# Optimization experiments

Hardware: AMD Instinct MI355X
Metric: run time of the kernel (lower is better)

## Reference

```python
import jax, jax.numpy as jnp
import numpy as np

N = 4096      # num nodes
E = 131072    # num edges
D = 128       # embed dim (in=out)
HID = 16      # kan hidden dim
G, K = 4, 3   # KAN grid_size / spline_order (GCN + FFN kans)
GA, KA = 2, 1 # attention KANLinear grid_size / spline_order
H, HD = 8, 16 # heads, head_dim

def make_grid(in_f, g, k):
    h = 2.0 / g
    pts = (np.arange(-k, g + k + 1) * h - 1.0).astype(np.float32)  # [g+2k+1]
    return jnp.asarray(np.tile(pts[None, :], (in_f, 1)))            # [in_f, g+2k+1]

GRID_D = make_grid(D, G, K)
GRID_H = make_grid(HID, G, K)
GRID_A = make_grid(D, GA, KA)

def b_splines(x, grid, k):
    # x: [n, in] -> B-spline bases [n, in, g+k] via Cox-de-Boor recursion
    x = x[:, :, None]
    g = grid[None]
    bases = ((x >= g[..., :-1]) & (x < g[..., 1:])).astype(x.dtype)
    for j in range(1, k + 1):
        bases = ((x - g[..., :-(j + 1)]) / (g[..., j:-1] - g[..., :-(j + 1)]) * bases[..., :-1]
                 + (g[..., j + 1:] - x) / (g[..., j + 1:] - g[..., 1:-j]) * bases[..., 1:])
    return bases

def kan_lin(x, bw, sw, grid, k, use_silu):
    base = jax.nn.silu(x) if use_silu else x
    return base @ bw.T + jnp.einsum('nig,oig->no', b_splines(x, grid, k), sw)

def ekan2(x, bw1, sw1, bw2, sw2):
    # eKAN with layers_hidden=[D, HID, D], SiLU base activation
    h = kan_lin(x, bw1, sw1, GRID_D, K, True)
    return kan_lin(h, bw2, sw2, GRID_H, K, True)

def layer_norm(h, s, b):
    m = jnp.mean(h, axis=-1, keepdims=True)
    v = jnp.var(h, axis=-1, keepdims=True)
    return (h - m) * jax.lax.rsqrt(v + 1e-5) * s + b

def setup_inputs() -> dict:
    key = jax.random.key(0)
    ks = jax.random.split(key, 20)
    r = lambda i, shape: jax.random.normal(ks[i], shape, jnp.float32) * 0.1
    return dict(
        x=jax.random.normal(ks[0], (N, D), jnp.float32),
        edge_index=jax.random.randint(ks[1], (2, E), 0, N),
        gcn_bw1=r(2, (HID, D)), gcn_sw1=r(3, (HID, D, G + K)),
        gcn_bw2=r(4, (D, HID)), gcn_sw2=r(5, (D, HID, G + K)),
        q_bw=r(6, (D, D)), q_sw=r(7, (D, D, GA + KA)),
        k_bw=r(8, (D, D)), k_sw=r(9, (D, D, GA + KA)),
        v_bw=r(10, (D, D)), v_sw=r(11, (D, D, GA + KA)),
        ffn_bw1=r(12, (HID, D)), ffn_sw1=r(13, (HID, D, G + K)),
        ffn_bw2=r(14, (D, HID)), ffn_sw2=r(15, (D, HID, G + K)),
        ln1_s=jnp.ones(D), ln1_b=jnp.zeros(D),
        ln2_s=jnp.ones(D), ln2_b=jnp.zeros(D),
        ln3_s=jnp.ones(D), ln3_b=jnp.zeros(D),
    )

def reference(x, edge_index, gcn_bw1, gcn_sw1, gcn_bw2, gcn_sw2,
              q_bw, q_sw, k_bw, k_sw, v_bw, v_sw,
              ffn_bw1, ffn_sw1, ffn_bw2, ffn_sw2,
              ln1_s, ln1_b, ln2_s, ln2_b, ln3_s, ln3_b):
    n = x.shape[0]
    # ---- local GCN-KAN branch: KAN(A_hat x) ----
    loops = jnp.arange(n)
    row = jnp.concatenate([edge_index[0], loops])  # sources (+ self-loops)
    col = jnp.concatenate([edge_index[1], loops])  # targets
    w = jnp.ones(row.shape[0], x.dtype)
    deg = jax.ops.segment_sum(w, row, num_segments=n)
    dis = jnp.where(deg > 0, deg ** -0.5, 0.0)
    norm = dis[row] * w * dis[col]
    agg = jax.ops.segment_sum(norm[:, None] * x[row], col, num_segments=n)  # [n, D]
    h_local = ekan2(agg, gcn_bw1, gcn_sw1, gcn_bw2, gcn_sw2)
    h_local = layer_norm(x + h_local, ln1_s, ln1_b)
    # ---- global KAN multi-head attention branch ----
    Q = kan_lin(x, q_bw, q_sw, GRID_A, KA, False).reshape(n, H, HD)
    Kv = kan_lin(x, k_bw, k_sw, GRID_A, KA, False).reshape(n, H, HD)
    V = kan_lin(x, v_bw, v_sw, GRID_A, KA, False).reshape(n, H, HD)
    scores = jnp.einsum('nhd,mhd->hnm', Q, Kv) / np.sqrt(HD)  # [H, n, n]
    attn = jax.nn.softmax(scores, axis=-1)
    h_attn = jnp.einsum('hnm,mhd->nhd', attn, V).reshape(n, D)
    h_attn = layer_norm(x + h_attn, ln2_s, ln2_b)
    # ---- combine + KAN feed-forward ----
    h = h_local + h_attn
    out = layer_norm(h + ekan2(h, ffn_bw1, ffn_sw1, ffn_bw2, ffn_sw2), ln3_s, ln3_b)
    return out
```

## Files before the change

### kernel.cpp

```cpp
#include <hip/hip_runtime.h>

typedef unsigned short u16;
typedef unsigned int u32;

#define D_ 128
#define HID_ 16
#define NH_ 8
#define HD_ 16
#define PSTRIDE 17

#define WE_W1G 0
#define WE_W2G 16384
#define WE_W1F 32768
#define WE_W2F 49152
#define WE_TOTAL 65536

#define KROW 24
#define VROW 136
#define PROW 40
#define HROW 136
#define AROW 1032
#define HVROW 132

#define QSCALE 0.3606737602222409f

typedef __attribute__((ext_vector_type(8))) short bfrag;
typedef __attribute__((ext_vector_type(4))) float ffrag;

#if defined(__has_builtin)
#if __has_builtin(__builtin_amdgcn_exp2f)
#define EXP2F(x) __builtin_amdgcn_exp2f(x)
#endif
#endif
#ifndef EXP2F
#define EXP2F(x) exp2f(x)
#endif


__device__ __forceinline__ float bf2f(u16 u) {
    union { u32 i; float f; } v; v.i = ((u32)u) << 16; return v.f;
}
__device__ __forceinline__ u16 f2bf(float f) {
    u32 x = __float_as_uint(f);
    u32 r = (x + 0x7fffu + ((x >> 16) & 1u)) >> 16;
    return (u16)r;
}
__device__ __forceinline__ float rdf(const void* p, int i, bool bf) {
    return bf ? bf2f(((const u16*)p)[i]) : ((const float*)p)[i];
}

__device__ __forceinline__ u32 probe_stat(const u16* p) {
    for (int i = 0; i < 128; i++) {
        u16 u = p[i];
        int e = (u >> 7) & 0xFF;
        int m = u & 0x7F;
        bool zero = (e == 0) && (m == 0);
        bool sane = zero || (e >= 97 && e <= 147);
        if (!sane) return 0u;
    }
    return 1u;
}

__global__ __launch_bounds__(256) void k_detect(const void* x,
                         const void* gbw1, const void* gsw1, const void* gbw2, const void* gsw2,
                         const void* qbw, const void* qsw, const void* kbw, const void* ksw,
                         const void* vbw, const void* vsw,
                         const void* fbw1, const void* fsw1, const void* fbw2, const void* fsw2,
                         const void* l1s, const void* l1b, const void* l2s, const void* l2b,
                         const void* l3s, const void* l3b,
                         u32* flags, int* __restrict__ cnt3, int N) {
    int t = threadIdx.x;
    const void* ptrs[21] = {x, gbw1, gsw1, gbw2, gsw2, qbw, qsw, kbw, ksw, vbw, vsw,
                            fbw1, fsw1, fbw2, fsw2, l1s, l1b, l2s, l2b, l3s, l3b};
    if (t < 21) {
        u32 f = 0;
        if (t == 15 || t == 17 || t == 19) {
            f = (((const u32*)ptrs[t])[0] != 0x3F800000u) ? 1u : 0u;
        } else if (t == 16 || t == 18 || t == 20) {
            f = 0;
        } else {
            f = probe_stat((const u16*)ptrs[t]);
        }
        flags[t] = f;
    }
    __syncthreads();
    if (t == 16 || t == 18 || t == 20) flags[t] = flags[t - 1];
    int tot = 3 * N;
    for (int i = t; i < tot; i += 256) cnt3[i] = 0;
}

__device__ __forceinline__ float cub_seg(float s) {
    if (s < 0.0f || s >= 4.0f) return 0.0f;
    if (s < 1.0f) return s * s * s * (1.0f / 6.0f);
    if (s < 2.0f) { float r = s - 1.0f; return (1.0f + 3.0f * r + 3.0f * r * r - 3.0f * r * r * r) * (1.0f / 6.0f); }
    if (s < 3.0f) { float r = s - 2.0f; return (4.0f - 6.0f * r * r + 3.0f * r * r * r) * (1.0f / 6.0f); }
    float q = 4.0f - s; return q * q * q * (1.0f / 6.0f);
}
__device__ __forceinline__ float lin_seg(float s) {
    if (s < 0.0f || s >= 2.0f) return 0.0f;
    return (s < 1.0f) ? s : (2.0f - s);
}

__device__ __forceinline__ uint4 feat8(float a) {
    float si = a / (1.0f + __expf(-a));
    float u = (a + 2.5f) * 2.0f;
    float b0 = cub_seg(u), b1 = cub_seg(u - 1.0f), b2 = cub_seg(u - 2.0f), b3 = cub_seg(u - 3.0f);
    float b4 = cub_seg(u - 4.0f), b5 = cub_seg(u - 5.0f), b6 = cub_seg(u - 6.0f);
    uint4 r;
    r.x = (u32)f2bf(si) | ((u32)f2bf(b0) << 16);
    r.y = (u32)f2bf(b1) | ((u32)f2bf(b2) << 16);
    r.z = (u32)f2bf(b3) | ((u32)f2bf(b4) << 16);
    r.w = (u32)f2bf(b5) | ((u32)f2bf(b6) << 16);
    return r;
}

__global__ __launch_bounds__(256) void k_setup(const void* __restrict__ x,
        const void* l1s, const void* l1b, const void* l2s,
        const void* l2b, const void* l3s, const void* l3b,
        const void* gbw1, const void* gsw1, const void* gbw2, const void* gsw2,
        const void* fbw1, const void* fsw1, const void* fbw2, const void* fsw2,
        const void* qbw, const void* qsw, const void* kbw, const void* ksw,
        const void* vbw, const void* vsw,
        const int* __restrict__ ei,
        const u32* __restrict__ flags,
        float* __restrict__ xin, float* __restrict__ lnp,
        u16* __restrict__ F,
        u16* __restrict__ Web, u16* __restrict__ Wb,
        int* __restrict__ cnt, int* __restrict__ degi,
        int N, int E) {
    int b = blockIdx.x;
    int convB = ((N * D_ + 768) + 255) >> 8;
    if (b < convB) {
        int i = b * 256 + threadIdx.x;
        if (i < N * D_) {
            float xv = rdf(x, i, flags[0] != 0);
            xin[i] = xv;
            float u = xv + 2.0f;
            u32 lo = (u32)f2bf(xv) | ((u32)f2bf(lin_seg(u)) << 16);
            u32 hi = (u32)f2bf(lin_seg(u - 1.0f)) | ((u32)f2bf(lin_seg(u - 2.0f)) << 16);
            ((uint2*)F)[i] = make_uint2(lo, hi);
        } else if (i < N * D_ + 768) {
            int j = i - N * D_;
            int sel = j >> 7, k = j & 127;
            const void* p = sel == 0 ? l1s : sel == 1 ? l1b : sel == 2 ? l2s
                         : sel == 3 ? l2b : sel == 4 ? l3s : l3b;
            lnp[j] = rdf(p, k, flags[15 + sel] != 0);
        }
    } else if (b < convB + 224) {
        int t = (b - convB) * 256 + threadIdx.x;
        if (t < 8192) {
            int seg = t >> 11, i = t & 2047;
            const void* bw = seg == 0 ? gbw1 : seg == 1 ? gbw2 : seg == 2 ? fbw1 : fbw2;
            const void* sw = seg == 0 ? gsw1 : seg == 1 ? gsw2 : seg == 2 ? fsw1 : fsw2;
            int fb = seg == 0 ? 1 : seg == 1 ? 3 : seg == 2 ? 11 : 13;
            bool bwbf = flags[fb] != 0, swbf = flags[fb + 1] != 0;
            u16* dst = Web + (size_t)seg * 16384 + (size_t)i * 8;
            dst[0] = f2bf(rdf(bw, i, bwbf));
#pragma unroll
            for (int g = 0; g < 7; g++) dst[1 + g] = f2bf(rdf(sw, i * 7 + g, swbf));
        } else if (t < 8192 + 49152) {
            int uu = t - 8192;
            int seg = uu >> 14, i = uu & 16383;
            const void* bw = seg == 0 ? qbw : seg == 1 ? kbw : vbw;
            const void* sw = seg == 0 ? qsw : seg == 1 ? ksw : vsw;
            int fb = 5 + seg * 2;
            bool bwbf = flags[fb] != 0, swbf = flags[fb + 1] != 0;
            float sc = (seg == 0) ? QSCALE : 1.0f;
            u16* dst = Wb + (size_t)seg * 65536 + (size_t)i * 4;
            dst[0] = f2bf(rdf(bw, i, bwbf) * sc);
#pragma unroll
            for (int g = 0; g < 3; g++) dst[1 + g] = f2bf(rdf(sw, i * 3 + g, swbf) * sc);
        }
    } else {
        int e = (b - convB - 224) * 256 + threadIdx.x;
        if (e < E) {
            atomicAdd(&degi[ei[e]], 1);
            atomicAdd(&cnt[ei[E + e]], 1);
        }
    }
}

__global__ __launch_bounds__(1024) void k_scan(const int* __restrict__ cnt,
                                               const int* __restrict__ degi,
                                               int* __restrict__ rowptr,
                                               float* __restrict__ dis, int N) {
    __shared__ int ws[16];
    int t = threadIdx.x;
    int base = t * 4;
    int a[4];
#pragma unroll
    for (int k = 0; k < 4; k++) a[k] = (base + k < N) ? cnt[base + k] : 0;
    int loc = a[0] + a[1] + a[2] + a[3];
    int pre = loc;
#pragma unroll
    for (int off = 1; off < 64; off <<= 1) {
        int v = __shfl_up(pre, off, 64);
        if ((t & 63) >= off) pre += v;
    }
    if ((t & 63) == 63) ws[t >> 6] = pre;
    __syncthreads();
    if (t < 64) {
        int v = (t < 16) ? ws[t] : 0;
#pragma unroll
        for (int off = 1; off < 16; off <<= 1) {
            int u = __shfl_up(v, off, 64);
            if (t >= off) v += u;
        }
        if (t < 16) ws[t] = v;
    }
    __syncthreads();
    int ex = pre - loc + ((t >= 64) ? ws[(t >> 6) - 1] : 0);
    int run = ex;
#pragma unroll
    for (int k = 0; k < 4; k++) {
        if (base + k < N) rowptr[base + k] = run;
        run += a[k];
    }
    if (t == 1023) rowptr[N] = ws[15];
#pragma unroll
    for (int k = 0; k < 4; k++)
        if (base + k < N) dis[base + k] = rsqrtf((float)degi[base + k] + 1.0f);
}

__global__ void k_fill(const int* __restrict__ ei, const int* __restrict__ rowptr,
                       int* __restrict__ fill, int* __restrict__ elist, int E) {
    int e = blockIdx.x * 256 + threadIdx.x;
    if (e < E) {
        int r = ei[e], c = ei[E + e];
        int pos = rowptr[c] + atomicAdd(&fill[c], 1);
        elist[pos] = r;
    }
}

__global__ __launch_bounds__(128) void k_gcn(const int* __restrict__ rowptr,
        const int* __restrict__ elist, const float* __restrict__ dis,
        const float* __restrict__ xin, u16* __restrict__ Afeat) {
    int c = blockIdx.x, t = threadIdx.x;
    __shared__ int ids[128];
    __shared__ float wsh[128];
    int beg = rowptr[c], end = rowptr[c + 1];
    float a0 = 0.0f, a1 = 0.0f, a2 = 0.0f, a3 = 0.0f;
    for (int j0 = beg; j0 < end; j0 += 128) {
        int cc = min(128, end - j0);
        __syncthreads();
        if (t < cc) {
            int rr = elist[j0 + t];
            ids[t] = rr;
            wsh[t] = dis[rr];
        }
        __syncthreads();
        int j = 0;
        for (; j + 4 <= cc; j += 4) {
            a0 += wsh[j]     * xin[(size_t)ids[j]     * D_ + t];
            a1 += wsh[j + 1] * xin[(size_t)ids[j + 1] * D_ + t];
            a2 += wsh[j + 2] * xin[(size_t)ids[j + 2] * D_ + t];
            a3 += wsh[j + 3] * xin[(size_t)ids[j + 3] * D_ + t];
        }
        for (; j < cc; j++) a0 += wsh[j] * xin[(size_t)ids[j] * D_ + t];
    }
    float dc = dis[c];
    float a = dc * (((a0 + a1) + (a2 + a3)) + dc * xin[(size_t)c * D_ + t]);
    ((uint4*)Afeat)[(size_t)c * D_ + t] = feat8(a);
}

#define EKAN_G1(APTR, ASTR, W1B) \
    if (ww == 0) { \
        const u16* ar = (APTR) + (size_t)l15 * (ASTR) + quad * 8; \
        const u16* br = (W1B) + (size_t)l15 * 1024 + quad * 8; \
        ffrag c0 = {0,0,0,0}, c1 = {0,0,0,0}, c2 = {0,0,0,0}, c3 = {0,0,0,0}; \
        for (int ks = 0; ks < 256; ks += 32) { \
            c0 = __builtin_amdgcn_mfma_f32_16x16x32_bf16(*(const bfrag*)(ar + ks),       *(const bfrag*)(br + ks),       c0, 0, 0, 0); \
            c1 = __builtin_amdgcn_mfma_f32_16x16x32_bf16(*(const bfrag*)(ar + 256 + ks), *(const bfrag*)(br + 256 + ks), c1, 0, 0, 0); \
            c2 = __builtin_amdgcn_mfma_f32_16x16x32_bf16(*(const bfrag*)(ar + 512 + ks), *(const bfrag*)(br + 512 + ks), c2, 0, 0, 0); \
            c3 = __builtin_amdgcn_mfma_f32_16x16x32_bf16(*(const bfrag*)(ar + 768 + ks), *(const bfrag*)(br + 768 + ks), c3, 0, 0, 0); \
        } \
        float e0 = (c0.x + c1.x) + (c2.x + c3.x); \
        float e1 = (c0.y + c1.y) + (c2.y + c3.y); \
        float e2 = (c0.z + c1.z) + (c2.z + c3.z); \
        float e3 = (c0.w + c1.w) + (c2.w + c3.w); \
        { uint4 fv = feat8(e0); *(uint4*)(&hfL[(quad * 4 + 0) * HROW + l15 * 8]) = fv; } \
        { uint4 fv = feat8(e1); *(uint4*)(&hfL[(quad * 4 + 1) * HROW + l15 * 8]) = fv; } \
        { uint4 fv = feat8(e2); *(uint4*)(&hfL[(quad * 4 + 2) * HROW + l15 * 8]) = fv; } \
        { uint4 fv = feat8(e3); *(uint4*)(&hfL[(quad * 4 + 3) * HROW + l15 * 8]) = fv; } \
    }

#define EK_TGET(RR, COMP, V0, V1, RES0EXPR, RES1EXPR) { \
    int row = quad * 4 + RR; \
    float r0 = (RES0EXPR); \
    float r1 = (RES1EXPR); \
    V0 = a0.COMP + r0; V1 = a1.COMP + r1; \
    float s1 = V0 + V1, s2 = V0 * V0 + V1 * V1; \
    s1 += __shfl_xor(s1, 1, 64); s2 += __shfl_xor(s2, 1, 64); \
    s1 += __shfl_xor(s1, 2, 64); s2 += __shfl_xor(s2, 2, 64); \
    s1 += __shfl_xor(s1, 4, 64); s2 += __shfl_xor(s2, 4, 64); \
    s1 += __shfl_xor(s1, 8, 64); s2 += __shfl_xor(s2, 8, 64); \
    if (l15 == 0) { redS[ww * 16 + row] = s1; redS[64 + ww * 16 + row] = s2; } }

#define EK_TOUT(RR, V0, V1, OUTP, BFO) { \
    int row = quad * 4 + RR; \
    float s1 = (redS[row] + redS[16 + row]) + (redS[32 + row] + redS[48 + row]); \
    float s2 = (redS[64 + row] + redS[80 + row]) + (redS[96 + row] + redS[112 + row]); \
    float mean = s1 * 0.0078125f; \
    float var = s2 * 0.0078125f - mean * mean; \
    float rs = rsqrtf(var + 1e-5f); \
    float y0 = (V0 - mean) * rs * ls0 + lb0; \
    float y1 = (V1 - mean) * rs * ls1 + lb1; \
    int node = node0 + row; \
    if (BFO) { \
        u16* ob = (u16*)(OUTP) + (size_t)node * 128; \
        ob[c0i] = f2bf(y0); ob[c1i] = f2bf(y1); \
    } else { \
        float* ob = (float*)(OUTP) + (size_t)node * 128; \
        ob[c0i] = y0; ob[c1i] = y1; \
    } }

#define EKAN_G2LN(W2B, LNS, LNB, RES0EXPR, RES1EXPR, OUTP, BFO) { \
    const u16* b0 = (W2B) + (size_t)l15 * 128 + quad * 8 + (size_t)(2 * ww) * 2048; \
    ffrag a0 = {0,0,0,0}, a1 = {0,0,0,0}; \
    for (int ks = 0; ks < 128; ks += 32) { \
        bfrag af = *(const bfrag*)(&hfL[l15 * HROW + quad * 8 + ks]); \
        a0 = __builtin_amdgcn_mfma_f32_16x16x32_bf16(af, *(const bfrag*)(b0 + ks),        a0, 0, 0, 0); \
        a1 = __builtin_amdgcn_mfma_f32_16x16x32_bf16(af, *(const bfrag*)(b0 + 2048 + ks), a1, 0, 0, 0); \
    } \
    int c0i = 32 * ww + l15, c1i = c0i + 16; \
    float ls0 = (LNS)[c0i], lb0 = (LNB)[c0i]; \
    float ls1 = (LNS)[c1i], lb1 = (LNB)[c1i]; \
    float v0r0, v0r1, v0r2, v0r3, v1r0, v1r1, v1r2, v1r3; \
    EK_TGET(0, x, v0r0, v1r0, RES0EXPR, RES1EXPR) \
    EK_TGET(1, y, v0r1, v1r1, RES0EXPR, RES1EXPR) \
    EK_TGET(2, z, v0r2, v1r2, RES0EXPR, RES1EXPR) \
    EK_TGET(3, w, v0r3, v1r3, RES0EXPR, RES1EXPR) \
    __syncthreads(); \
    EK_TOUT(0, v0r0, v1r0, OUTP, BFO) \
    EK_TOUT(1, v0r1, v1r1, OUTP, BFO) \
    EK_TOUT(2, v0r2, v1r2, OUTP, BFO) \
    EK_TOUT(3, v0r3, v1r3, OUTP, BFO) }

__global__ __launch_bounds__(256) void k_ekan4(const u16* __restrict__ A,
        const u16* __restrict__ W1b, const u16* __restrict__ W2b,
        const float* __restrict__ resid,
        const float* __restrict__ lns, const float* __restrict__ lnb,
        float* __restrict__ outp, int N) {
    __shared__ u16 hfL[16 * HROW];
    __shared__ float redS[128];
    int mt = blockIdx.x, t = threadIdx.x;
    int ww = t >> 6, lane = t & 63, quad = lane >> 4, l15 = lane & 15;
    int node0 = mt * 16;
    const u16* Ab = A + (size_t)node0 * 1024;
    EKAN_G1(Ab, 1024, W1b)
    __syncthreads();
    EKAN_G2LN(W2b, lns, lnb,
              resid[(size_t)(node0 + row) * 128 + c0i],
              resid[(size_t)(node0 + row) * 128 + c1i],
              outp, false)
    (void)lane;
}

#define QKV_STORE(ACC, TL) { \
    int col = cg * 48 + (TL) * 16 + l15; \
    int mat = col >> 7, idx = col & 127; \
    u16* dstb = (mat == 0) ? Qb : (mat == 1) ? Kb : Vb; \
    size_t base = (size_t)(idx >> 4) * N * HD_ + (size_t)(idx & 15); \
    dstb[base + (size_t)(rowb + 0) * HD_] = f2bf(ACC.x); \
    dstb[base + (size_t)(rowb + 1) * HD_] = f2bf(ACC.y); \
    dstb[base + (size_t)(rowb + 2) * HD_] = f2bf(ACC.z); \
    dstb[base + (size_t)(rowb + 3) * HD_] = f2bf(ACC.w); \
}

__global__ __launch_bounds__(64) void k_qkv5(const u16* __restrict__ F,
        const u16* __restrict__ Wb,
        u16* __restrict__ Qb, u16* __restrict__ Kb, u16* __restrict__ Vb, int N) {
    int mt = blockIdx.x, cg = blockIdx.y;
    int lane = threadIdx.x, quad = lane >> 4, l15 = lane & 15;
    const u16* arow = F + (size_t)(mt * 16 + l15) * 512 + quad * 8;
    const u16* b0r = Wb + (size_t)(cg * 48 + l15) * 512 + quad * 8;
    const u16* b1r = b0r + 16 * 512;
    const u16* b2r = b0r + 32 * 512;
    ffrag a0 = {0, 0, 0, 0}, a1 = {0, 0, 0, 0}, a2 = {0, 0, 0, 0};
#pragma unroll
    for (int ks = 0; ks < 512; ks += 32) {
        bfrag af = *(const bfrag*)(arow + ks);
        bfrag bf0 = *(const bfrag*)(b0r + ks);
        bfrag bf1 = *(const bfrag*)(b1r + ks);
        bfrag bf2 = *(const bfrag*)(b2r + ks);
        a0 = __builtin_amdgcn_mfma_f32_16x16x32_bf16(af, bf0, a0, 0, 0, 0);
        a1 = __builtin_amdgcn_mfma_f32_16x16x32_bf16(af, bf1, a1, 0, 0, 0);
        a2 = __builtin_amdgcn_mfma_f32_16x16x32_bf16(af, bf2, a2, 0, 0, 0);
    }
    int rowb = mt * 16 + quad * 4;
    QKV_STORE(a0, 0)
    QKV_STORE(a1, 1)
    QKV_STORE(a2, 2)
}

#define ATTN_SCORE(QF, LACC, PBT) { \
    ffrag zz = {0.0f, 0.0f, 0.0f, 0.0f}; \
    ffrag s0 = __builtin_amdgcn_mfma_f32_16x16x32_bf16(QF, kf0, zz, 0, 0, 0); \
    ffrag s1 = __builtin_amdgcn_mfma_f32_16x16x32_bf16(QF, kf1, zz, 0, 0, 0); \
    float a0 = EXP2F(s0.x), a1 = EXP2F(s0.y), a2 = EXP2F(s0.z), a3 = EXP2F(s0.w); \
    float b0 = EXP2F(s1.x), b1 = EXP2F(s1.y), b2 = EXP2F(s1.z), b3 = EXP2F(s1.w); \
    LACC.x += a0 + b0; LACC.y += a1 + b1; LACC.z += a2 + b2; LACC.w += a3 + b3; \
    u32* pw = (u32*)PBT; \
    pw[(quad * 4 + 0) * (PROW / 2) + l15] = (__float_as_uint(a0) >> 16) | (__float_as_uint(b0) & 0xFFFF0000u); \
    pw[(quad * 4 + 1) * (PROW / 2) + l15] = (__float_as_uint(a1) >> 16) | (__float_as_uint(b1) & 0xFFFF0000u); \
    pw[(quad * 4 + 2) * (PROW / 2) + l15] = (__float_as_uint(a2) >> 16) | (__float_as_uint(b2) & 0xFFFF0000u); \
    pw[(quad * 4 + 3) * (PROW / 2) + l15] = (__float_as_uint(a3) >> 16) | (__float_as_uint(b3) & 0xFFFF0000u); \
}

#define ATTN_PV(OACC, PBT) { \
    bfrag pf = *(const bfrag*)(&PBT[l15 * PROW + quad * 8]); \
    OACC = __builtin_amdgcn_mfma_f32_16x16x32_bf16(pf, vf, OACC, 0, 0, 0); \
}

#define STORE_TILE(OACC, LACC, TL) { \
    int q0 = qtb + (TL) * 16 + quad * 4; \
    float* pp; \
    pp = part + ((size_t)(h * N + q0 + 0) * SPLIT + s) * PSTRIDE; \
    pp[1 + l15] = OACC.x; if (l15 == 0) pp[0] = LACC.x; \
    pp = part + ((size_t)(h * N + q0 + 1) * SPLIT + s) * PSTRIDE; \
    pp[1 + l15] = OACC.y; if (l15 == 0) pp[0] = LACC.y; \
    pp = part + ((size_t)(h * N + q0 + 2) * SPLIT + s) * PSTRIDE; \
    pp[1 + l15] = OACC.z; if (l15 == 0) pp[0] = LACC.z; \
    pp = part + ((size_t)(h * N + q0 + 3) * SPLIT + s) * PSTRIDE; \
    pp[1 + l15] = OACC.w; if (l15 == 0) pp[0] = LACC.w; \
}

__global__ __launch_bounds__(256) void k_attn9(const u16* __restrict__ Qb,
        const u16* __restrict__ Kb, const u16* __restrict__ Vb,
        float* __restrict__ part, int N, int SPLIT) {
    int s = blockIdx.x, qb = blockIdx.y, h = blockIdx.z;
    int t = threadIdx.x;
    int w = t >> 6, lane = t & 63, quad = lane >> 4, l15 = lane & 15;
    __shared__ u16 ldsK[128 * KROW + 16];
    __shared__ u16 ldsVt[16 * VROW];
    __shared__ u16 ldsP[4][4][16 * PROW];

    const u16* qrow = Qb + (size_t)h * N * HD_;
    const u16* krow = Kb + (size_t)h * N * HD_;
    const u16* vrow = Vb + (size_t)h * N * HD_;

    for (int i = t; i < (128 * KROW + 16) / 2; i += 256) ((u32*)ldsK)[i] = 0;

    int qtb = qb * 256 + w * 64;
    bfrag qz = {0, 0, 0, 0, 0, 0, 0, 0};
    bfrag qf0 = qz, qf1 = qz, qf2 = qz, qf3 = qz;
    if (quad < 2) {
        qf0 = *(const bfrag*)(qrow + (size_t)(qtb + 0 * 16 + l15) * HD_ + quad * 8);
        qf1 = *(const bfrag*)(qrow + (size_t)(qtb + 1 * 16 + l15) * HD_ + quad * 8);
        qf2 = *(const bfrag*)(qrow + (size_t)(qtb + 2 * 16 + l15) * HD_ + quad * 8);
        qf3 = *(const bfrag*)(qrow + (size_t)(qtb + 3 * 16 + l15) * HD_ + quad * 8);
    }

    ffrag o0 = {0, 0, 0, 0}, o1 = {0, 0, 0, 0}, o2 = {0, 0, 0, 0}, o3 = {0, 0, 0, 0};
    ffrag L0 = {0, 0, 0, 0}, L1 = {0, 0, 0, 0}, L2 = {0, 0, 0, 0}, L3 = {0, 0, 0, 0};
    u16* pb0 = &ldsP[w][0][0];
    u16* pb1 = &ldsP[w][1][0];
    u16* pb2 = &ldsP[w][2][0];
    u16* pb3 = &ldsP[w][3][0];

    int keys = N / SPLIT;
    int kstart0 = s * keys;
    for (int kst = 0; kst < keys; kst += 128) {
        int kg = kstart0 + kst;
        __syncthreads();
        if (t < 128) {
            const uint4* src = (const uint4*)(krow + (size_t)(kg + t) * HD_);
            uint4 a = src[0], b = src[1];
            *(uint4*)(&ldsK[t * KROW]) = a;
            *(uint4*)(&ldsK[t * KROW + 8]) = b;
        } else {
            int key = t - 128;
            const uint4* src = (const uint4*)(vrow + (size_t)(kg + key) * HD_);
            uint4 a = src[0], b = src[1];
            ldsVt[0 * VROW + key] = (u16)(a.x);  ldsVt[1 * VROW + key] = (u16)(a.x >> 16);
            ldsVt[2 * VROW + key] = (u16)(a.y);  ldsVt[3 * VROW + key] = (u16)(a.y >> 16);
            ldsVt[4 * VROW + key] = (u16)(a.z);  ldsVt[5 * VROW + key] = (u16)(a.z >> 16);
            ldsVt[6 * VROW + key] = (u16)(a.w);  ldsVt[7 * VROW + key] = (u16)(a.w >> 16);
            ldsVt[8 * VROW + key] = (u16)(b.x);  ldsVt[9 * VROW + key] = (u16)(b.x >> 16);
            ldsVt[10 * VROW + key] = (u16)(b.y); ldsVt[11 * VROW + key] = (u16)(b.y >> 16);
            ldsVt[12 * VROW + key] = (u16)(b.z); ldsVt[13 * VROW + key] = (u16)(b.z >> 16);
            ldsVt[14 * VROW + key] = (u16)(b.w); ldsVt[15 * VROW + key] = (u16)(b.w >> 16);
        }
        __syncthreads();
#pragma unroll
        for (int koff = 0; koff < 128; koff += 32) {
            bfrag kf0 = *(const bfrag*)(&ldsK[(koff + 2 * l15) * KROW + quad * 8]);
            bfrag kf1 = *(const bfrag*)(&ldsK[(koff + 2 * l15 + 1) * KROW + quad * 8]);
            bfrag vf = *(const bfrag*)(&ldsVt[l15 * VROW + koff + quad * 8]);
            ATTN_SCORE(qf0, L0, pb0)
            ATTN_SCORE(qf1, L1, pb1)
            ATTN_SCORE(qf2, L2, pb2)
            ATTN_SCORE(qf3, L3, pb3)
            __asm__ volatile("s_waitcnt lgkmcnt(0)" ::: "memory");
            ATTN_PV(o0, pb0)
            ATTN_PV(o1, pb1)
            ATTN_PV(o2, pb2)
            ATTN_PV(o3, pb3)
        }
    }

#pragma unroll
    for (int off = 1; off < 16; off <<= 1) {
        L0.x += __shfl_xor(L0.x, off, 64); L0.y += __shfl_xor(L0.y, off, 64);
        L0.z += __shfl_xor(L0.z, off, 64); L0.w += __shfl_xor(L0.w, off, 64);
        L1.x += __shfl_xor(L1.x, off, 64); L1.y += __shfl_xor(L1.y, off, 64);
        L1.z += __shfl_xor(L1.z, off, 64); L1.w += __shfl_xor(L1.w, off, 64);
        L2.x += __shfl_xor(L2.x, off, 64); L2.y += __shfl_xor(L2.y, off, 64);
        L2.z += __shfl_xor(L2.z, off, 64); L2.w += __shfl_xor(L2.w, off, 64);
        L3.x += __shfl_xor(L3.x, off, 64); L3.y += __shfl_xor(L3.y, off, 64);
        L3.z += __shfl_xor(L3.z, off, 64); L3.w += __shfl_xor(L3.w, off, 64);
    }
    STORE_TILE(o0, L0, 0)
    STORE_TILE(o1, L1, 1)
    STORE_TILE(o2, L2, 2)
    STORE_TILE(o3, L3, 3)
}

__global__ __launch_bounds__(256) void k_comb_ekan(
        const float* __restrict__ part,
        const float* __restrict__ xin, const float* __restrict__ hl,
        const float* __restrict__ lnp,
        const u16* __restrict__ W1b, const u16* __restrict__ W2b,
        void* __restrict__ outp, const u32* __restrict__ flags,
        int N, int SPLIT) {
    __shared__ u16 hfA[16 * AROW];
    __shared__ u16 hfL[16 * HROW];
    __shared__ float redS[128];
    __shared__ float hvL[16 * HVROW];
    __shared__ float redA[4], redB[4];
    int mt = blockIdx.x, t = threadIdx.x;
    int half = t >> 7, tl = t & 127;
    int ww = t >> 6, lane = t & 63, quad = lane >> 4, l15 = lane & 15;
    int hh = tl >> 4, dd = tl & 15;
    int node0 = mt * 16;
#pragma unroll 1
    for (int i = 0; i < 16; i += 2) {
        int node = node0 + i + half;
        float L = 0.0f, O = 0.0f;
        for (int ss = 0; ss < SPLIT; ss++) {
            const float* ps = part + ((size_t)(hh * N + node) * SPLIT + ss) * PSTRIDE;
            L += ps[0];
            O += ps[1 + dd];
        }
        float r = xin[(size_t)node * D_ + tl] + O / L;
        float s1 = r, s2 = r * r;
#pragma unroll
        for (int off = 1; off < 64; off <<= 1) {
            s1 += __shfl_xor(s1, off, 64);
            s2 += __shfl_xor(s2, off, 64);
        }
        if ((t & 63) == 0) { redA[ww] = s1; redB[ww] = s2; }
        __syncthreads();
        float S1 = redA[half * 2] + redA[half * 2 + 1];
        float S2 = redB[half * 2] + redB[half * 2 + 1];
        float mean = S1 * 0.0078125f;
        float var = S2 * 0.0078125f - mean * mean;
        float rs = rsqrtf(var + 1e-5f);
        float y2 = (r - mean) * rs * lnp[256 + tl] + lnp[384 + tl];
        float hvv = hl[(size_t)node * D_ + tl] + y2;
        hvL[(i + half) * HVROW + tl] = hvv;
        *(uint4*)(&hfA[(i + half) * AROW + tl * 8]) = feat8(hvv);
        __syncthreads();
    }
    bool bfo = flags[0] != 0;
    EKAN_G1(hfA, AROW, W1b)
    __syncthreads();
    EKAN_G2LN(W2b, lnp + 512, lnp + 640,
              hvL[row * HVROW + c0i],
              hvL[row * HVROW + c1i],
              outp, bfo)
    (void)lane;
}

extern "C" void kernel_launch(void* const* d_in, const int* in_sizes, int n_in,
                              void* d_out, int out_size, void* d_ws, size_t ws_size,
                              hipStream_t stream) {
    const void* x = d_in[0];
    const int* ei = (const int*)d_in[1];
    const void* gbw1 = d_in[2];
    const void* gsw1 = d_in[3];
    const void* gbw2 = d_in[4];
    const void* gsw2 = d_in[5];
    const void* qbw = d_in[6];
    const void* qsw = d_in[7];
    const void* kbw = d_in[8];
    const void* ksw = d_in[9];
    const void* vbw = d_in[10];
    const void* vsw = d_in[11];
    const void* fbw1 = d_in[12];
    const void* fsw1 = d_in[13];
    const void* fbw2 = d_in[14];
    const void* fsw2 = d_in[15];
    const void* ln1s = d_in[16];
    const void* ln1b = d_in[17];
    const void* ln2s = d_in[18];
    const void* ln2b = d_in[19];
    const void* ln3s = d_in[20];
    const void* ln3b = d_in[21];

    const int N = in_sizes[0] / D_;
    const int E = in_sizes[1] / 2;
    const size_t ND = (size_t)N * D_;

    float* wf = (float*)d_ws;
    u32* flags = (u32*)wf;
    float* lnp = wf + 32;
    float* dis = wf + 800;
    float* xin = dis + N;
    float* hl  = xin + ND;
    u16* Web = (u16*)(hl + ND);
    u16* Wb  = Web + WE_TOTAL;
    u16* F   = Wb + 196608;
    u16* Qb  = F + (size_t)N * 512;
    u16* Kb  = Qb + ND;
    u16* Vb  = Kb + ND;
    u16* Afeat = Vb + ND;
    int* cnt    = (int*)(Afeat + (size_t)N * 1024);
    int* fill   = cnt + N;
    int* degi   = fill + N;
    int* rowptr = degi + N;
    int* elist  = rowptr + N + 1;
    float* part = (float*)(elist + E);

    size_t baseBytes = (size_t)((char*)part - (char*)d_ws);
    int SPLIT = 8;
    if (baseBytes + (size_t)NH_ * N * 8 * PSTRIDE * 4 > ws_size) SPLIT = 4;
    if (baseBytes + (size_t)NH_ * N * 4 * PSTRIDE * 4 > ws_size) SPLIT = 2;

    int convB = ((N * D_ + 768) + 255) >> 8;
    int countB = (E + 255) / 256;

    k_detect<<<1, 256, 0, stream>>>(x, gbw1, gsw1, gbw2, gsw2, qbw, qsw, kbw, ksw,
                                    vbw, vsw, fbw1, fsw1, fbw2, fsw2,
                                    ln1s, ln1b, ln2s, ln2b, ln3s, ln3b, flags, cnt, N);
    k_setup<<<convB + 224 + countB, 256, 0, stream>>>(
        x, ln1s, ln1b, ln2s, ln2b, ln3s, ln3b,
        gbw1, gsw1, gbw2, gsw2, fbw1, fsw1, fbw2, fsw2,
        qbw, qsw, kbw, ksw, vbw, vsw,
        ei, flags, xin, lnp, F, Web, Wb, cnt, degi, N, E);
    k_qkv5<<<dim3(N / 16, 8), 64, 0, stream>>>(F, Wb, Qb, Kb, Vb, N);
    k_scan<<<1, 1024, 0, stream>>>(cnt, degi, rowptr, dis, N);
    k_fill<<<countB, 256, 0, stream>>>(ei, rowptr, fill, elist, E);
    k_gcn<<<N, 128, 0, stream>>>(rowptr, elist, dis, xin, Afeat);
    k_ekan4<<<N / 16, 256, 0, stream>>>(Afeat, Web + WE_W1G, Web + WE_W2G, xin,
                                        lnp + 0, lnp + 128, hl, N);
    k_attn9<<<dim3(SPLIT, N / 256, NH_), 256, 0, stream>>>(Qb, Kb, Vb, part, N, SPLIT);
    k_comb_ekan<<<N / 16, 256, 0, stream>>>(part, xin, hl, lnp,
                                            Web + WE_W1F, Web + WE_W2F,
                                            d_out, flags, N, SPLIT);
}
```

Measured before the change: 249.2 us.

## Split combine+FFN eKAN into separate kernels and spread first GEMM across four waves

The first eKAN GEMM, previously done by a single wave per block, is split across all four waves by K-slices and reduced through shared memory. The fused combine+FFN kernel is split into a per-node combine/layernorm kernel that writes hv and spline features to global memory, followed by a reuse of the generic eKAN kernel. This raises parallelism in the combine stage and the GEMM at the cost of an extra launch, an extra sync, and a global round trip of the feature buffer.

```diff
diff --git a/kernel.cpp b/kernel.cpp
--- a/kernel.cpp
+++ b/kernel.cpp
@@ -19,8 +19,6 @@
 #define VROW 136
 #define PROW 40
 #define HROW 136
-#define AROW 1032
-#define HVROW 132
 
 #define QSCALE 0.3606737602222409f
 
@@ -99,6 +97,15 @@
 __device__ __forceinline__ float lin_seg(float s) {
     if (s < 0.0f || s >= 2.0f) return 0.0f;
     return (s < 1.0f) ? s : (2.0f - s);
+}
+
+__device__ __forceinline__ float bsum(float v, float* tmp) {
+#pragma unroll
+    for (int off = 1; off < 64; off <<= 1) v += __shfl_xor(v, off, 64);
+    __syncthreads();
+    if ((threadIdx.x & 63) == 0) tmp[threadIdx.x >> 6] = v;
+    __syncthreads();
+    return tmp[0] + tmp[1];
 }
 
 __device__ __forceinline__ uint4 feat8(float a) {
@@ -263,26 +270,27 @@
     ((uint4*)Afeat)[(size_t)c * D_ + t] = feat8(a);
 }
 
-#define EKAN_G1(APTR, ASTR, W1B) \
+#define EKAN_G1_4W(APTR, ASTR, W1B) { \
+    const u16* ar = (APTR) + (size_t)l15 * (ASTR) + (size_t)ww * 256 + quad * 8; \
+    const u16* br = (W1B) + (size_t)l15 * 1024 + (size_t)ww * 256 + quad * 8; \
+    ffrag c0 = {0,0,0,0}, c1 = {0,0,0,0}; \
+    for (int ks = 0; ks < 128; ks += 32) { \
+        c0 = __builtin_amdgcn_mfma_f32_16x16x32_bf16(*(const bfrag*)(ar + ks),       *(const bfrag*)(br + ks),       c0, 0, 0, 0); \
+        c1 = __builtin_amdgcn_mfma_f32_16x16x32_bf16(*(const bfrag*)(ar + 128 + ks), *(const bfrag*)(br + 128 + ks), c1, 0, 0, 0); \
+    } \
+    redG[ww][lane] = make_float4(c0.x + c1.x, c0.y + c1.y, c0.z + c1.z, c0.w + c1.w); \
+    __syncthreads(); \
     if (ww == 0) { \
-        const u16* ar = (APTR) + (size_t)l15 * (ASTR) + quad * 8; \
-        const u16* br = (W1B) + (size_t)l15 * 1024 + quad * 8; \
-        ffrag c0 = {0,0,0,0}, c1 = {0,0,0,0}, c2 = {0,0,0,0}, c3 = {0,0,0,0}; \
-        for (int ks = 0; ks < 256; ks += 32) { \
-            c0 = __builtin_amdgcn_mfma_f32_16x16x32_bf16(*(const bfrag*)(ar + ks),       *(const bfrag*)(br + ks),       c0, 0, 0, 0); \
-            c1 = __builtin_amdgcn_mfma_f32_16x16x32_bf16(*(const bfrag*)(ar + 256 + ks), *(const bfrag*)(br + 256 + ks), c1, 0, 0, 0); \
-            c2 = __builtin_amdgcn_mfma_f32_16x16x32_bf16(*(const bfrag*)(ar + 512 + ks), *(const bfrag*)(br + 512 + ks), c2, 0, 0, 0); \
-            c3 = __builtin_amdgcn_mfma_f32_16x16x32_bf16(*(const bfrag*)(ar + 768 + ks), *(const bfrag*)(br + 768 + ks), c3, 0, 0, 0); \
-        } \
-        float e0 = (c0.x + c1.x) + (c2.x + c3.x); \
-        float e1 = (c0.y + c1.y) + (c2.y + c3.y); \
-        float e2 = (c0.z + c1.z) + (c2.z + c3.z); \
-        float e3 = (c0.w + c1.w) + (c2.w + c3.w); \
+        float4 p0 = redG[0][lane], p1 = redG[1][lane], p2 = redG[2][lane], p3 = redG[3][lane]; \
+        float e0 = (p0.x + p1.x) + (p2.x + p3.x); \
+        float e1 = (p0.y + p1.y) + (p2.y + p3.y); \
+        float e2 = (p0.z + p1.z) + (p2.z + p3.z); \
+        float e3 = (p0.w + p1.w) + (p2.w + p3.w); \
         { uint4 fv = feat8(e0); *(uint4*)(&hfL[(quad * 4 + 0) * HROW + l15 * 8]) = fv; } \
         { uint4 fv = feat8(e1); *(uint4*)(&hfL[(quad * 4 + 1) * HROW + l15 * 8]) = fv; } \
         { uint4 fv = feat8(e2); *(uint4*)(&hfL[(quad * 4 + 2) * HROW + l15 * 8]) = fv; } \
         { uint4 fv = feat8(e3); *(uint4*)(&hfL[(quad * 4 + 3) * HROW + l15 * 8]) = fv; } \
-    }
+    } }
 
 #define EK_TGET(RR, COMP, V0, V1, RES0EXPR, RES1EXPR) { \
     int row = quad * 4 + RR; \
@@ -340,20 +348,21 @@
         const u16* __restrict__ W1b, const u16* __restrict__ W2b,
         const float* __restrict__ resid,
         const float* __restrict__ lns, const float* __restrict__ lnb,
-        float* __restrict__ outp, int N) {
+        void* __restrict__ outp, const u32* __restrict__ flags, int fin, int N) {
     __shared__ u16 hfL[16 * HROW];
     __shared__ float redS[128];
+    __shared__ float4 redG[4][64];
     int mt = blockIdx.x, t = threadIdx.x;
     int ww = t >> 6, lane = t & 63, quad = lane >> 4, l15 = lane & 15;
     int node0 = mt * 16;
     const u16* Ab = A + (size_t)node0 * 1024;
-    EKAN_G1(Ab, 1024, W1b)
+    bool bfo = (fin != 0) && (flags[0] != 0);
+    EKAN_G1_4W(Ab, 1024, W1b)
     __syncthreads();
     EKAN_G2LN(W2b, lns, lnb,
               resid[(size_t)(node0 + row) * 128 + c0i],
               resid[(size_t)(node0 + row) * 128 + c1i],
-              outp, false)
-    (void)lane;
+              outp, bfo)
 }
 
 #define QKV_STORE(ACC, TL) { \
@@ -516,60 +525,28 @@
     STORE_TILE(o3, L3, 3)
 }
 
-__global__ __launch_bounds__(256) void k_comb_ekan(
-        const float* __restrict__ part,
+__global__ __launch_bounds__(128) void k_comb(const float* __restrict__ part,
         const float* __restrict__ xin, const float* __restrict__ hl,
-        const float* __restrict__ lnp,
-        const u16* __restrict__ W1b, const u16* __restrict__ W2b,
-        void* __restrict__ outp, const u32* __restrict__ flags,
-        int N, int SPLIT) {
-    __shared__ u16 hfA[16 * AROW];
-    __shared__ u16 hfL[16 * HROW];
-    __shared__ float redS[128];
-    __shared__ float hvL[16 * HVROW];
-    __shared__ float redA[4], redB[4];
-    int mt = blockIdx.x, t = threadIdx.x;
-    int half = t >> 7, tl = t & 127;
-    int ww = t >> 6, lane = t & 63, quad = lane >> 4, l15 = lane & 15;
-    int hh = tl >> 4, dd = tl & 15;
-    int node0 = mt * 16;
-#pragma unroll 1
-    for (int i = 0; i < 16; i += 2) {
-        int node = node0 + i + half;
-        float L = 0.0f, O = 0.0f;
-        for (int ss = 0; ss < SPLIT; ss++) {
-            const float* ps = part + ((size_t)(hh * N + node) * SPLIT + ss) * PSTRIDE;
-            L += ps[0];
-            O += ps[1 + dd];
-        }
-        float r = xin[(size_t)node * D_ + tl] + O / L;
-        float s1 = r, s2 = r * r;
-#pragma unroll
-        for (int off = 1; off < 64; off <<= 1) {
-            s1 += __shfl_xor(s1, off, 64);
-            s2 += __shfl_xor(s2, off, 64);
-        }
-        if ((t & 63) == 0) { redA[ww] = s1; redB[ww] = s2; }
-        __syncthreads();
-        float S1 = redA[half * 2] + redA[half * 2 + 1];
-        float S2 = redB[half * 2] + redB[half * 2 + 1];
-        float mean = S1 * 0.0078125f;
-        float var = S2 * 0.0078125f - mean * mean;
-        float rs = rsqrtf(var + 1e-5f);
-        float y2 = (r - mean) * rs * lnp[256 + tl] + lnp[384 + tl];
-        float hvv = hl[(size_t)node * D_ + tl] + y2;
-        hvL[(i + half) * HVROW + tl] = hvv;
-        *(uint4*)(&hfA[(i + half) * AROW + tl * 8]) = feat8(hvv);
-        __syncthreads();
-    }
-    bool bfo = flags[0] != 0;
-    EKAN_G1(hfA, AROW, W1b)
-    __syncthreads();
-    EKAN_G2LN(W2b, lnp + 512, lnp + 640,
-              hvL[row * HVROW + c0i],
-              hvL[row * HVROW + c1i],
-              outp, bfo)
-    (void)lane;
+        const float* __restrict__ lnp, float* __restrict__ hv,
+        u16* __restrict__ Afeat, int N, int SPLIT) {
+    int n = blockIdx.x, t = threadIdx.x;
+    __shared__ float red[128];
+    int h = t >> 4, d = t & 15;
+    float L = 0.0f, O = 0.0f;
+    for (int ss = 0; ss < SPLIT; ss++) {
+        const float* ps = part + ((size_t)(h * N + n) * SPLIT + ss) * PSTRIDE;
+        L += ps[0];
+        O += ps[1 + d];
+    }
+    float ha = O / L;
+    float r = xin[(size_t)n * D_ + t] + ha;
+    float mean = bsum(r, red) * (1.0f / 128.0f);
+    float c = r - mean;
+    float var = bsum(c * c, red) * (1.0f / 128.0f);
+    float y2 = c * rsqrtf(var + 1e-5f) * lnp[256 + t] + lnp[384 + t];
+    float hvv = hl[(size_t)n * D_ + t] + y2;
+    hv[(size_t)n * D_ + t] = hvv;
+    ((uint4*)Afeat)[(size_t)n * D_ + t] = feat8(hvv);
 }
 
 extern "C" void kernel_launch(void* const* d_in, const int* in_sizes, int n_in,
@@ -608,7 +585,8 @@
     float* dis = wf + 800;
     float* xin = dis + N;
     float* hl  = xin + ND;
-    u16* Web = (u16*)(hl + ND);
+    float* hv  = hl + ND;
+    u16* Web = (u16*)(hv + ND);
     u16* Wb  = Web + WE_TOTAL;
     u16* F   = Wb + 196608;
     u16* Qb  = F + (size_t)N * 512;
@@ -643,9 +621,9 @@
     k_fill<<<countB, 256, 0, stream>>>(ei, rowptr, fill, elist, E);
     k_gcn<<<N, 128, 0, stream>>>(rowptr, elist, dis, xin, Afeat);
     k_ekan4<<<N / 16, 256, 0, stream>>>(Afeat, Web + WE_W1G, Web + WE_W2G, xin,
-                                        lnp + 0, lnp + 128, hl, N);
+                                        lnp + 0, lnp + 128, hl, flags, 0, N);
     k_attn9<<<dim3(SPLIT, N / 256, NH_), 256, 0, stream>>>(Qb, Kb, Vb, part, N, SPLIT);
-    k_comb_ekan<<<N / 16, 256, 0, stream>>>(part, xin, hl, lnp,
-                                            Web + WE_W1F, Web + WE_W2F,
-                                            d_out, flags, N, SPLIT);
-}
+    k_comb<<<N, 128, 0, stream>>>(part, xin, hl, lnp, hv, Afeat, N, SPLIT);
+    k_ekan4<<<N / 16, 256, 0, stream>>>(Afeat, Web + WE_W1F, Web + WE_W2F, hv,
+                                        lnp + 512, lnp + 640, d_out, flags, 1, N);
+}
```

Result: faster. 235.4 us (-5.6%).
